# Optimization experiments

Hardware: AMD Instinct MI355X
Metric: run time of the kernel (lower is better)

The kernel has to match this reference:

```python
import jax, jax.numpy as jnp
import numpy as np

B, T, E, H = 8, 2048, 1024, 128

def setup_inputs() -> dict:
    key = jax.random.key(0)
    kx, kq, kk, kv = jax.random.split(key, 4)
    return {
        "X": jax.random.normal(kx, (B, T, E), dtype=jnp.float32),
        "Wq": jax.random.normal(kq, (E, H), dtype=jnp.float32) * (E ** -0.5),
        "Wk": jax.random.normal(kk, (E, H), dtype=jnp.float32) * (E ** -0.5),
        "Wv": jax.random.normal(kv, (E, H), dtype=jnp.float32) * (E ** -0.5),
    }

def reference(X, Wq, Wk, Wv):
    # X: [B, T, E]; Wq/Wk/Wv: [E, H]
    q = X @ Wq  # [B, T, H]
    k = X @ Wk  # [B, T, H]
    v = X @ Wv  # [B, T, H]
    t = X.shape[1]
    scale = float(X.shape[-1]) ** 0.5  # NOTE: source scales by sqrt(embedding_size)
    w = jnp.einsum("bqh,bkh->bqk", q, k) / scale  # [B, T, T]
    mask = jnp.tril(jnp.ones((t, t), dtype=bool))  # causal tril buffer
    w = jnp.where(mask[None, :, :], w, -jnp.inf)
    # NOTE: source applies softmax over dim=1 (the query axis), faithfully reproduced
    w = jax.nn.softmax(w, axis=1)
    # dropout p=0.0 -> identity
    return jnp.einsum("bqk,bkh->bqh", w, v)  # [B, T, H]
```

## Files before the change

### kernel.cpp

```cpp
#include <hip/hip_runtime.h>
#include <hip/hip_bf16.h>
#include <stdint.h>

#define B_ 8
#define T_ 2048
#define E_ 1024
#define H_ 128
#define BT_ (B_*T_)

typedef unsigned short u16;
typedef unsigned int u32;
typedef __attribute__((ext_vector_type(4))) unsigned short u16x4;
typedef __attribute__((ext_vector_type(8))) short short8;
typedef __attribute__((ext_vector_type(4))) float f32x4;

#define MFMA_BF16(a,b,c) __builtin_amdgcn_mfma_f32_16x16x32_bf16((a),(b),(c),0,0,0)

#define SBAR() do { __builtin_amdgcn_sched_barrier(0); __builtin_amdgcn_s_barrier(); __builtin_amdgcn_sched_barrier(0); } while(0)
#define WAITL0() asm volatile("s_waitcnt lgkmcnt(0)" ::: "memory")

__device__ __forceinline__ u16 bf16u(float f) {
  union { float f; unsigned u; } v; v.f = f;
  unsigned r = v.u + 0x7FFFu + ((v.u >> 16) & 1u);
  return (u16)(r >> 16);
}
__device__ __forceinline__ float ubf16(u16 u) {
  union { unsigned u; float f; } v; v.u = ((unsigned)u) << 16; return v.f;
}

__device__ __forceinline__ void gl16(const void* g, void* l) {
  __builtin_amdgcn_global_load_lds(
      (const __attribute__((address_space(1))) void*)g,
      (__attribute__((address_space(3))) void*)l, 16, 0, 0);
}

template<int R, int CB, bool SWZ>
__device__ __forceinline__ void stage_tile(const char* g, int gstride, char* lds) {
  const int lane = threadIdx.x & 63;
  const int wid  = threadIdx.x >> 6;
  constexpr int LPR   = CB / 16;
  constexpr int RPC   = 1024 / CB;
  constexpr int CALLS = (R * CB) / 1024;
  constexpr int CPW   = CALLS / 4;
#pragma unroll
  for (int c = 0; c < CPW; ++c) {
    const int call = wid * CPW + c;
    const int r0   = call * RPC;
    const int row  = r0 + lane / LPR;
    int s = lane % LPR;
    if (SWZ) s = s ^ (row & 7);
    gl16(g + (size_t)row * gstride + s * 16, lds + (size_t)r0 * CB);
  }
}

__device__ __forceinline__ short8 fragr(const u16* lds, int row, int colu16, int CBu) {
  const int slot = (colu16 >> 3) ^ (row & 7);
  return *(const short8*)&lds[(size_t)row * CBu + (slot << 3)];
}

__global__ void k_prep(const float* __restrict__ X, u16* __restrict__ Xb,
                       const float* __restrict__ Wq, const float* __restrict__ Wk,
                       const float* __restrict__ Wv, u16* __restrict__ Wt,
                       float* __restrict__ colsum) {
  const int gidx = blockIdx.x * 256 + threadIdx.x;
  const int n4 = BT_ * E_ / 4;
  for (int i = gidx; i < n4; i += gridDim.x * 256) {
    float4 v = ((const float4*)X)[i];
    u16x4 o;
    o.x = bf16u(v.x); o.y = bf16u(v.y); o.z = bf16u(v.z); o.w = bf16u(v.w);
    ((u16x4*)Xb)[i] = o;
  }
  if (gidx < BT_) colsum[gidx] = 0.f;
  if (gidx < 384 * 1024) {
    int r = gidx >> 10;
    int e = gidx & 1023;
    int i = r >> 7;
    int h = r & 127;
    const float* W = (i == 0) ? Wq : (i == 1) ? Wk : Wv;
    float v = W[(size_t)e * 128 + h];
    if (i == 0) v *= 0.03125f;
    Wt[gidx] = bf16u(v);
  }
}

__global__ __launch_bounds__(256) void k_qkv_gemm(const u16* __restrict__ Xb, const u16* __restrict__ Wt,
                                                  u16* __restrict__ Qs, u16* __restrict__ Kb,
                                                  u16* __restrict__ Vt) {
  __shared__ __align__(16) u16 As[2][128 * 64];
  __shared__ __align__(16) u16 Bs[2][128 * 64];
  const int m0   = blockIdx.x * 128;
  const int nsel = blockIdx.y;
  const int n0   = nsel * 128;
  const int lane = threadIdx.x & 63;
  const int wid  = threadIdx.x >> 6;
  const int ln = lane & 15, h4 = lane >> 4;
  const int wm = (wid >> 1) * 64, wn = (wid & 1) * 64;
  f32x4 acc[4][4] = {};

  auto stage = [&](int t, int buf) {
    stage_tile<128, 128, true>((const char*)(Xb + (size_t)m0 * E_ + t * 64), E_ * 2, (char*)As[buf]);
    stage_tile<128, 128, true>((const char*)(Wt + (size_t)n0 * E_ + t * 64), E_ * 2, (char*)Bs[buf]);
  };
  stage(0, 0);
  for (int t = 0; t < 16; ++t) {
    const int cur = t & 1;
    if (t < 15) stage(t + 1, cur ^ 1);
    if (t < 15) asm volatile("s_waitcnt vmcnt(8)" ::: "memory");
    else        asm volatile("s_waitcnt vmcnt(0)" ::: "memory");
    SBAR();
#pragma unroll
    for (int kk = 0; kk < 2; ++kk) {
      short8 a[4], b[4];
#pragma unroll
      for (int mf = 0; mf < 4; ++mf)
        a[mf] = fragr(As[cur], wm + mf * 16 + ln, kk * 32 + h4 * 8, 64);
#pragma unroll
      for (int nf = 0; nf < 4; ++nf)
        b[nf] = fragr(Bs[cur], wn + nf * 16 + ln, kk * 32 + h4 * 8, 64);
#pragma unroll
      for (int mf = 0; mf < 4; ++mf)
#pragma unroll
        for (int nf = 0; nf < 4; ++nf)
          acc[mf][nf] = MFMA_BF16(a[mf], b[nf], acc[mf][nf]);
    }
    WAITL0();
    SBAR();
  }
#pragma unroll
  for (int mf = 0; mf < 4; ++mf)
#pragma unroll
    for (int nf = 0; nf < 4; ++nf)
#pragma unroll
      for (int i = 0; i < 4; ++i) {
        int r = m0 + wm + mf * 16 + h4 * 4 + i;
        int c = wn + nf * 16 + ln;
        u16 u = bf16u(acc[mf][nf][i]);
        if (nsel == 0)      Qs[(size_t)r * H_ + c] = u;
        else if (nsel == 1) Kb[(size_t)r * H_ + c] = u;
        else {
          int bb = r >> 11, tt = r & (T_ - 1);
          Vt[((size_t)bb * H_ + c) * T_ + tt] = u;
        }
      }
}

__global__ __launch_bounds__(256) void k_score(const u16* __restrict__ Qs, const u16* __restrict__ Kb,
                                               u16* __restrict__ P, float* __restrict__ colsum) {
  __shared__ __align__(16) u16 Kf[128 * 128];
  const int c = blockIdx.x, a = blockIdx.y, b = blockIdx.z;
  const int lo = (c * 17) >> 3, hi = ((c + 1) * 17) >> 3;
  const int lane = threadIdx.x & 63, wid = threadIdx.x >> 6;
  const int ln = lane & 15, h4 = lane >> 4;
  const int wq0 = wid * 32;
  const bool evenlane = !(ln & 1);
  int curqt = -1;
  short8 qa[2][4];
  for (int t = lo; t < hi; ++t) {
    const int qt = (t <= a) ? a : 15 - a;
    const int kt = (t <= a) ? t : t - (a + 1);
    stage_tile<128, 256, true>((const char*)(Kb + ((size_t)b * T_ + kt * 128) * H_), H_ * 2, (char*)Kf);
    if (qt != curqt) {
#pragma unroll
      for (int mf = 0; mf < 2; ++mf)
#pragma unroll
        for (int kk = 0; kk < 4; ++kk)
          qa[mf][kk] = *(const short8*)&Qs[((size_t)b * T_ + qt * 128 + wq0 + mf * 16 + ln) * H_ + kk * 32 + h4 * 8];
      curqt = qt;
    }
    asm volatile("s_waitcnt vmcnt(0)" ::: "memory");
    SBAR();

    f32x4 acc[2][8] = {};
#pragma unroll
    for (int kk = 0; kk < 4; ++kk) {
#pragma unroll
      for (int nf = 0; nf < 8; ++nf) {
        short8 bv = fragr(Kf, nf * 16 + ln, kk * 32 + h4 * 8, 128);
#pragma unroll
        for (int mf = 0; mf < 2; ++mf)
          acc[mf][nf] = MFMA_BF16(qa[mf][kk], bv, acc[mf][nf]);
      }
    }

    const bool diag = (qt == kt);
#pragma unroll
    for (int nf = 0; nf < 8; ++nf) {
      float s = 0.f;
      const int k = nf * 16 + ln;
#pragma unroll
      for (int mf = 0; mf < 2; ++mf) {
#pragma unroll
        for (int i = 0; i < 4; ++i) {
          const int q = wq0 + mf * 16 + h4 * 4 + i;
          float w = __expf(acc[mf][nf][i]);
          if (diag && q < k) w = 0.f;
          acc[mf][nf][i] = w;
          s += w;
        }
      }
      s += __shfl_xor(s, 16);
      s += __shfl_xor(s, 32);
      if (h4 == 0) atomicAdd(&colsum[(size_t)b * T_ + kt * 128 + nf * 16 + ln], s);
    }

    u16* ptile = P + (((size_t)b * 136 + (size_t)qt * (qt + 1) / 2 + kt) << 14);
#pragma unroll
    for (int mf = 0; mf < 2; ++mf)
#pragma unroll
      for (int nf = 0; nf < 8; ++nf) {
        f32x4 v = acc[mf][nf];
        f32x4 pv_;
#pragma unroll
        for (int i = 0; i < 4; ++i) pv_[i] = __shfl_xor(v[i], 1);
#pragma unroll
        for (int j = 0; j < 2; ++j) {
          const int i = evenlane ? j : (2 + j);
          const float flo = evenlane ? v[i] : pv_[i];
          const float fhh = evenlane ? pv_[i] : v[i];
          const u32 pk = (u32)bf16u(flo) | ((u32)bf16u(fhh) << 16);
          const int row = wq0 + mf * 16 + h4 * 4 + i;
          const int kc  = nf * 16 + (ln & ~1);
          *(u32*)((char*)ptile + row * 256 + kc * 2) = pk;
        }
      }
    WAITL0();
    SBAR();
  }
}

__global__ void k_finalize_v(const float* __restrict__ colsum, u16* __restrict__ Vt) {
  const int i8 = blockIdx.x * 256 + threadIdx.x;
  const int b  = i8 >> 15;
  const int r  = i8 & 32767;
  const int h  = r >> 8;
  const int t8 = r & 255;
  u16* p = Vt + ((size_t)b * H_ + h) * T_ + t8 * 8;
  const float* csp = colsum + (size_t)b * T_ + t8 * 8;
  short8 v = *(short8*)p;
  short8 o;
#pragma unroll
  for (int j = 0; j < 8; ++j) {
    float f = ubf16((u16)v[j]) / csp[j];
    o[j] = (short)bf16u(f);
  }
  *(short8*)p = o;
}

__global__ __launch_bounds__(256) void k_pv(const u16* __restrict__ P, const u16* __restrict__ Vt,
                                            float* __restrict__ out) {
  __shared__ __align__(16) u16 Pt[2][128 * 128];
  __shared__ __align__(16) u16 Vs[2][16 * 128];
  const int id = blockIdx.x;
  const int hq = id >> 6;
  const int b  = (id >> 3) & 7;
  const int a  = id & 7;
  const int lane = threadIdx.x & 63, wid = threadIdx.x >> 6;
  const int ln = lane & 15, h4 = lane >> 4;
  const int wq0 = wid * 32;

  auto stage = [&](int t, int buf) {
    const int qt = (t <= a) ? a : 15 - a;
    const int kt = (t <= a) ? t : t - (a + 1);
    const u16* ptile = P + (((size_t)b * 136 + (size_t)qt * (qt + 1) / 2 + kt) << 14);
    stage_tile<128, 256, true>((const char*)ptile, 256, (char*)Pt[buf]);
    stage_tile<16, 256, true>((const char*)(Vt + ((size_t)b * H_ + hq * 16) * T_ + kt * 128), T_ * 2, (char*)Vs[buf]);
  };

  stage(0, 0);
  f32x4 acc[2] = {};
  for (int t = 0; t < 17; ++t) {
    const int cur = t & 1;
    if (t < 16) stage(t + 1, cur ^ 1);
    if (t < 16) asm volatile("s_waitcnt vmcnt(9)" ::: "memory");
    else        asm volatile("s_waitcnt vmcnt(0)" ::: "memory");
    SBAR();
#pragma unroll
    for (int kk = 0; kk < 4; ++kk) {
      short8 bv = fragr(Vs[cur], ln, kk * 32 + h4 * 8, 128);
#pragma unroll
      for (int mf = 0; mf < 2; ++mf) {
        short8 av = fragr(Pt[cur], wq0 + mf * 16 + ln, kk * 32 + h4 * 8, 128);
        acc[mf] = MFMA_BF16(av, bv, acc[mf]);
      }
    }
    if (t == a || t == 16) {
      const int qt = (t == a) ? a : 15 - a;
#pragma unroll
      for (int mf = 0; mf < 2; ++mf) {
#pragma unroll
        for (int i = 0; i < 4; ++i) {
          const int q = qt * 128 + wq0 + mf * 16 + h4 * 4 + i;
          out[((size_t)b * T_ + q) * H_ + hq * 16 + ln] = acc[mf][i];
        }
        acc[mf] = (f32x4){0.f, 0.f, 0.f, 0.f};
      }
    }
    WAITL0();
    SBAR();
  }
}

extern "C" void kernel_launch(void* const* d_in, const int* in_sizes, int n_in,
                              void* d_out, int out_size, void* d_ws, size_t ws_size,
                              hipStream_t stream) {
  const float* X  = (const float*)d_in[0];
  const float* Wq = (const float*)d_in[1];
  const float* Wk = (const float*)d_in[2];
  const float* Wv = (const float*)d_in[3];
  float* out = (float*)d_out;
  char* ws = (char*)d_ws;

  u16 *Xb, *Wt, *Qs, *Kb, *Vt, *Pb;
  float* colsum;
  if (ws_size >= 82640896ULL) {
    Xb = (u16*)(ws + 0);
    Wt = (u16*)(ws + 33554432);
    Qs = (u16*)(ws + 34340864);
    Kb = (u16*)(ws + 38535168);
    Vt = (u16*)(ws + 42729472);
    colsum = (float*)(ws + 46923776);
    Pb = (u16*)(ws + 46989312);
  } else {
    Qs = (u16*)(ws + 0);
    Kb = (u16*)(ws + 4194304);
    Vt = (u16*)(ws + 8388608);
    colsum = (float*)(ws + 12582912);
    Pb = (u16*)(ws + 12648448);
    Xb = (u16*)(ws + 12648448);
    Wt = (u16*)(ws + 46202880);
  }

  k_prep<<<2048, 256, 0, stream>>>(X, Xb, Wq, Wk, Wv, Wt, colsum);
  k_qkv_gemm<<<dim3(128, 3), 256, 0, stream>>>(Xb, Wt, Qs, Kb, Vt);
  k_score<<<dim3(8, 8, 8), 256, 0, stream>>>(Qs, Kb, Pb, colsum);
  k_finalize_v<<<1024, 256, 0, stream>>>(colsum, Vt);
  k_pv<<<512, 256, 0, stream>>>(Pb, Vt, out);
}
```

Measured before the change: 180.0 us.

## Fuse X bf16 conversion into QKV GEMM and merge attention phases cooperatively

```diff
diff --git a/kernel.cpp b/kernel.cpp
--- a/kernel.cpp
+++ b/kernel.cpp
@@ -1,5 +1,6 @@
 #include <hip/hip_runtime.h>
 #include <hip/hip_bf16.h>
+#include <hip/hip_cooperative_groups.h>
 #include <stdint.h>
 
 #define B_ 8
@@ -58,18 +59,10 @@
   return *(const short8*)&lds[(size_t)row * CBu + (slot << 3)];
 }
 
-__global__ void k_prep(const float* __restrict__ X, u16* __restrict__ Xb,
-                       const float* __restrict__ Wq, const float* __restrict__ Wk,
+__global__ void k_prep(const float* __restrict__ Wq, const float* __restrict__ Wk,
                        const float* __restrict__ Wv, u16* __restrict__ Wt,
                        float* __restrict__ colsum) {
   const int gidx = blockIdx.x * 256 + threadIdx.x;
-  const int n4 = BT_ * E_ / 4;
-  for (int i = gidx; i < n4; i += gridDim.x * 256) {
-    float4 v = ((const float4*)X)[i];
-    u16x4 o;
-    o.x = bf16u(v.x); o.y = bf16u(v.y); o.z = bf16u(v.z); o.w = bf16u(v.w);
-    ((u16x4*)Xb)[i] = o;
-  }
   if (gidx < BT_) colsum[gidx] = 0.f;
   if (gidx < 384 * 1024) {
     int r = gidx >> 10;
@@ -83,71 +76,107 @@
   }
 }
 
-__global__ __launch_bounds__(256) void k_qkv_gemm(const u16* __restrict__ Xb, const u16* __restrict__ Wt,
-                                                  u16* __restrict__ Qs, u16* __restrict__ Kb,
-                                                  u16* __restrict__ Vt) {
-  __shared__ __align__(16) u16 As[2][128 * 64];
-  __shared__ __align__(16) u16 Bs[2][128 * 64];
-  const int m0   = blockIdx.x * 128;
-  const int nsel = blockIdx.y;
-  const int n0   = nsel * 128;
-  const int lane = threadIdx.x & 63;
-  const int wid  = threadIdx.x >> 6;
+__global__ __launch_bounds__(256, 1) void k_qkv(const float* __restrict__ X,
+    const u16* __restrict__ Wt, u16* __restrict__ Qs, u16* __restrict__ Kb,
+    u16* __restrict__ Vt) {
+  __shared__ __align__(16) u16 As[2][64 * 64];
+  __shared__ __align__(16) u16 Bs[2][384 * 64];
+  const int m0 = blockIdx.x * 64;
+  const int tid = threadIdx.x;
+  const int lane = tid & 63, wid = tid >> 6;
   const int ln = lane & 15, h4 = lane >> 4;
-  const int wm = (wid >> 1) * 64, wn = (wid & 1) * 64;
-  f32x4 acc[4][4] = {};
-
-  auto stage = [&](int t, int buf) {
-    stage_tile<128, 128, true>((const char*)(Xb + (size_t)m0 * E_ + t * 64), E_ * 2, (char*)As[buf]);
-    stage_tile<128, 128, true>((const char*)(Wt + (size_t)n0 * E_ + t * 64), E_ * 2, (char*)Bs[buf]);
-  };
-  stage(0, 0);
-  for (int t = 0; t < 16; ++t) {
-    const int cur = t & 1;
-    if (t < 15) stage(t + 1, cur ^ 1);
-    if (t < 15) asm volatile("s_waitcnt vmcnt(8)" ::: "memory");
-    else        asm volatile("s_waitcnt vmcnt(0)" ::: "memory");
-    SBAR();
+  const int wr = (wid >> 1) * 32, wc = (wid & 1) * 192;
+  const int ar_r = tid >> 2, ar_c = tid & 3;
+  const float* xrow = X + (size_t)(m0 + ar_r) * E_ + ar_c * 16;
+  f32x4 acc[2][12] = {};
+  float4 arA[4], arB[4];
+
+  auto issueA = [&](int t, float4* ar) {
+    const float4* src = (const float4*)(xrow + t * 64);
+#pragma unroll
+    for (int j = 0; j < 4; ++j) ar[j] = src[j];
+  };
+  auto writeA = [&](int buf, const float4* ar) {
+    u16 tmp[16];
+#pragma unroll
+    for (int j = 0; j < 4; ++j) {
+      tmp[4*j+0] = bf16u(ar[j].x); tmp[4*j+1] = bf16u(ar[j].y);
+      tmp[4*j+2] = bf16u(ar[j].z); tmp[4*j+3] = bf16u(ar[j].w);
+    }
+    const int s0 = ar_c * 2;
+    u16* base = As[buf] + ar_r * 64;
+    *(short8*)(base + (((s0    ) ^ (ar_r & 7)) << 3)) = *(const short8*)&tmp[0];
+    *(short8*)(base + (((s0 + 1) ^ (ar_r & 7)) << 3)) = *(const short8*)&tmp[8];
+  };
+  auto stageB = [&](int t, int buf) {
+    stage_tile<384, 128, true>((const char*)(Wt + t * 64), 2048, (char*)Bs[buf]);
+  };
+  auto compute = [&](int c) {
 #pragma unroll
     for (int kk = 0; kk < 2; ++kk) {
-      short8 a[4], b[4];
-#pragma unroll
-      for (int mf = 0; mf < 4; ++mf)
-        a[mf] = fragr(As[cur], wm + mf * 16 + ln, kk * 32 + h4 * 8, 64);
-#pragma unroll
-      for (int nf = 0; nf < 4; ++nf)
-        b[nf] = fragr(Bs[cur], wn + nf * 16 + ln, kk * 32 + h4 * 8, 64);
-#pragma unroll
-      for (int mf = 0; mf < 4; ++mf)
-#pragma unroll
-        for (int nf = 0; nf < 4; ++nf)
+      short8 a[2], b[12];
+#pragma unroll
+      for (int mf = 0; mf < 2; ++mf)
+        a[mf] = fragr(As[c], wr + mf * 16 + ln, kk * 32 + h4 * 8, 64);
+#pragma unroll
+      for (int nf = 0; nf < 12; ++nf)
+        b[nf] = fragr(Bs[c], wc + nf * 16 + ln, kk * 32 + h4 * 8, 64);
+#pragma unroll
+      for (int mf = 0; mf < 2; ++mf)
+#pragma unroll
+        for (int nf = 0; nf < 12; ++nf)
           acc[mf][nf] = MFMA_BF16(a[mf], b[nf], acc[mf][nf]);
     }
-    WAITL0();
-    SBAR();
-  }
-#pragma unroll
-  for (int mf = 0; mf < 4; ++mf)
-#pragma unroll
-    for (int nf = 0; nf < 4; ++nf)
+  };
+
+  issueA(0, arA);
+  stageB(0, 0);
+  issueA(1, arB);
+  writeA(0, arA);
+  asm volatile("s_waitcnt vmcnt(4)" ::: "memory");
+  WAITL0(); SBAR();
+
+  auto body = [&](int t, float4* issDst, const float4* cvtSrc) {
+    const int c = t & 1;
+    if (t < 15) stageB(t + 1, c ^ 1);
+    if (t < 14) issueA(t + 2, issDst);
+    compute(c);
+    if (t < 15) {
+      writeA(c ^ 1, cvtSrc);
+      if (t < 14) asm volatile("s_waitcnt vmcnt(4)" ::: "memory");
+      else        asm volatile("s_waitcnt vmcnt(0)" ::: "memory");
+      WAITL0(); SBAR();
+    }
+  };
+  for (int tt = 0; tt < 16; tt += 2) {
+    body(tt,     arA, arB);
+    body(tt + 1, arB, arA);
+  }
+
+#pragma unroll
+  for (int mf = 0; mf < 2; ++mf)
+#pragma unroll
+    for (int nf = 0; nf < 12; ++nf) {
+      const int cg = wc + nf * 16 + ln;
 #pragma unroll
       for (int i = 0; i < 4; ++i) {
-        int r = m0 + wm + mf * 16 + h4 * 4 + i;
-        int c = wn + nf * 16 + ln;
-        u16 u = bf16u(acc[mf][nf][i]);
-        if (nsel == 0)      Qs[(size_t)r * H_ + c] = u;
-        else if (nsel == 1) Kb[(size_t)r * H_ + c] = u;
+        const int r = m0 + wr + mf * 16 + h4 * 4 + i;
+        const u16 u = bf16u(acc[mf][nf][i]);
+        if (cg < 128)      Qs[(size_t)r * H_ + cg] = u;
+        else if (cg < 256) Kb[(size_t)r * H_ + (cg - 128)] = u;
         else {
-          int bb = r >> 11, tt = r & (T_ - 1);
-          Vt[((size_t)bb * H_ + c) * T_ + tt] = u;
+          const int bb = r >> 11, t2 = r & (T_ - 1);
+          Vt[((size_t)bb * H_ + (cg - 256)) * T_ + t2] = u;
         }
       }
-}
-
-__global__ __launch_bounds__(256) void k_score(const u16* __restrict__ Qs, const u16* __restrict__ Kb,
-                                               u16* __restrict__ P, float* __restrict__ colsum) {
-  __shared__ __align__(16) u16 Kf[128 * 128];
-  const int c = blockIdx.x, a = blockIdx.y, b = blockIdx.z;
+    }
+}
+
+
+__device__ void phase_score(int wg, u16* lds, const u16* Qs, const u16* Kb,
+                            u16* P, float* colsum) {
+  u16* Kf = lds;
+  const int c = wg >> 6, a = (wg >> 3) & 7, b = wg & 7;
   const int lo = (c * 17) >> 3, hi = ((c + 1) * 17) >> 3;
   const int lane = threadIdx.x & 63, wid = threadIdx.x >> 6;
   const int ln = lane & 15, h4 = lane >> 4;
@@ -228,32 +257,32 @@
   }
 }
 
-__global__ void k_finalize_v(const float* __restrict__ colsum, u16* __restrict__ Vt) {
-  const int i8 = blockIdx.x * 256 + threadIdx.x;
-  const int b  = i8 >> 15;
-  const int r  = i8 & 32767;
-  const int h  = r >> 8;
-  const int t8 = r & 255;
-  u16* p = Vt + ((size_t)b * H_ + h) * T_ + t8 * 8;
-  const float* csp = colsum + (size_t)b * T_ + t8 * 8;
-  short8 v = *(short8*)p;
-  short8 o;
-#pragma unroll
-  for (int j = 0; j < 8; ++j) {
-    float f = ubf16((u16)v[j]) / csp[j];
-    o[j] = (short)bf16u(f);
-  }
-  *(short8*)p = o;
-}
-
-__global__ __launch_bounds__(256) void k_pv(const u16* __restrict__ P, const u16* __restrict__ Vt,
-                                            float* __restrict__ out) {
-  __shared__ __align__(16) u16 Pt[2][128 * 128];
-  __shared__ __align__(16) u16 Vs[2][16 * 128];
-  const int id = blockIdx.x;
-  const int hq = id >> 6;
-  const int b  = (id >> 3) & 7;
-  const int a  = id & 7;
+__device__ void phase_finalize(int wg, const float* colsum, u16* Vt) {
+  for (int i8 = wg * 256 + threadIdx.x; i8 < BT_ * H_ / 8; i8 += 512 * 256) {
+    const int b  = i8 >> 15;
+    const int r  = i8 & 32767;
+    const int h  = r >> 8;
+    const int t8 = r & 255;
+    u16* p = Vt + ((size_t)b * H_ + h) * T_ + t8 * 8;
+    const float* csp = colsum + (size_t)b * T_ + t8 * 8;
+    short8 v = *(short8*)p;
+    short8 o;
+#pragma unroll
+    for (int j = 0; j < 8; ++j) {
+      float f = ubf16((u16)v[j]) / csp[j];
+      o[j] = (short)bf16u(f);
+    }
+    *(short8*)p = o;
+  }
+}
+
+__device__ void phase_pv(int wg, u16* lds, const u16* P, const u16* Vt,
+                         float* out) {
+  u16* Pt0 = lds;
+  u16* Pt1 = lds + 16384;
+  u16* Vs0 = lds + 32768;
+  u16* Vs1 = lds + 34816;
+  const int hq = wg >> 6, b = (wg >> 3) & 7, a = wg & 7;
   const int lane = threadIdx.x & 63, wid = threadIdx.x >> 6;
   const int ln = lane & 15, h4 = lane >> 4;
   const int wq0 = wid * 32;
@@ -262,8 +291,8 @@
     const int qt = (t <= a) ? a : 15 - a;
     const int kt = (t <= a) ? t : t - (a + 1);
     const u16* ptile = P + (((size_t)b * 136 + (size_t)qt * (qt + 1) / 2 + kt) << 14);
-    stage_tile<128, 256, true>((const char*)ptile, 256, (char*)Pt[buf]);
-    stage_tile<16, 256, true>((const char*)(Vt + ((size_t)b * H_ + hq * 16) * T_ + kt * 128), T_ * 2, (char*)Vs[buf]);
+    stage_tile<128, 256, true>((const char*)ptile, 256, (char*)(buf ? Pt1 : Pt0));
+    stage_tile<16, 256, true>((const char*)(Vt + ((size_t)b * H_ + hq * 16) * T_ + kt * 128), T_ * 2, (char*)(buf ? Vs1 : Vs0));
   };
 
   stage(0, 0);
@@ -274,12 +303,14 @@
     if (t < 16) asm volatile("s_waitcnt vmcnt(9)" ::: "memory");
     else        asm volatile("s_waitcnt vmcnt(0)" ::: "memory");
     SBAR();
+    const u16* Ptc = cur ? Pt1 : Pt0;
+    const u16* Vsc = cur ? Vs1 : Vs0;
 #pragma unroll
     for (int kk = 0; kk < 4; ++kk) {
-      short8 bv = fragr(Vs[cur], ln, kk * 32 + h4 * 8, 128);
+      short8 bv = fragr(Vsc, ln, kk * 32 + h4 * 8, 128);
 #pragma unroll
       for (int mf = 0; mf < 2; ++mf) {
-        short8 av = fragr(Pt[cur], wq0 + mf * 16 + ln, kk * 32 + h4 * 8, 128);
+        short8 av = fragr(Ptc, wq0 + mf * 16 + ln, kk * 32 + h4 * 8, 128);
         acc[mf] = MFMA_BF16(av, bv, acc[mf]);
       }
     }
@@ -298,6 +329,36 @@
     WAITL0();
     SBAR();
   }
+}
+
+__global__ __launch_bounds__(256, 2) void k_fused(const u16* Qs, const u16* Kb,
+    u16* P, float* colsum, u16* Vt, float* out) {
+  __shared__ __align__(16) u16 lds[36864];
+  cooperative_groups::grid_group grid = cooperative_groups::this_grid();
+  const int wg = blockIdx.x;
+  phase_score(wg, lds, Qs, Kb, P, colsum);
+  asm volatile("s_waitcnt vmcnt(0) lgkmcnt(0)" ::: "memory");
+  __threadfence();
+  grid.sync();
+  phase_finalize(wg, colsum, Vt);
+  asm volatile("s_waitcnt vmcnt(0) lgkmcnt(0)" ::: "memory");
+  __threadfence();
+  grid.sync();
+  phase_pv(wg, lds, P, Vt, out);
+}
+
+__global__ __launch_bounds__(256, 2) void k_score_only(const u16* Qs, const u16* Kb,
+    u16* P, float* colsum) {
+  __shared__ __align__(16) u16 lds[16384];
+  phase_score(blockIdx.x, lds, Qs, Kb, P, colsum);
+}
+__global__ void k_finalize_only(const float* colsum, u16* Vt) {
+  phase_finalize(blockIdx.x, colsum, Vt);
+}
+__global__ __launch_bounds__(256, 2) void k_pv_only(const u16* P, const u16* Vt,
+    float* out) {
+  __shared__ __align__(16) u16 lds[36864];
+  phase_pv(blockIdx.x, lds, P, Vt, out);
 }
 
 extern "C" void kernel_launch(void* const* d_in, const int* in_sizes, int n_in,
@@ -310,29 +371,23 @@
   float* out = (float*)d_out;
   char* ws = (char*)d_ws;
 
-  u16 *Xb, *Wt, *Qs, *Kb, *Vt, *Pb;
-  float* colsum;
-  if (ws_size >= 82640896ULL) {
-    Xb = (u16*)(ws + 0);
-    Wt = (u16*)(ws + 33554432);
-    Qs = (u16*)(ws + 34340864);
-    Kb = (u16*)(ws + 38535168);
-    Vt = (u16*)(ws + 42729472);
-    colsum = (float*)(ws + 46923776);
-    Pb = (u16*)(ws + 46989312);
-  } else {
-    Qs = (u16*)(ws + 0);
-    Kb = (u16*)(ws + 4194304);
-    Vt = (u16*)(ws + 8388608);
-    colsum = (float*)(ws + 12582912);
-    Pb = (u16*)(ws + 12648448);
-    Xb = (u16*)(ws + 12648448);
-    Wt = (u16*)(ws + 46202880);
-  }
-
-  k_prep<<<2048, 256, 0, stream>>>(X, Xb, Wq, Wk, Wv, Wt, colsum);
-  k_qkv_gemm<<<dim3(128, 3), 256, 0, stream>>>(Xb, Wt, Qs, Kb, Vt);
-  k_score<<<dim3(8, 8, 8), 256, 0, stream>>>(Qs, Kb, Pb, colsum);
-  k_finalize_v<<<1024, 256, 0, stream>>>(colsum, Vt);
-  k_pv<<<512, 256, 0, stream>>>(Pb, Vt, out);
-}
+  u16*   Wt     = (u16*)(ws + 0);
+  u16*   Qs     = (u16*)(ws + 786432);
+  u16*   Kb     = (u16*)(ws + 4980736);
+  u16*   Vt     = (u16*)(ws + 9175040);
+  float* colsum = (float*)(ws + 13369344);
+  u16*   Pb     = (u16*)(ws + 13434880);
+
+  k_prep<<<1536, 256, 0, stream>>>(Wq, Wk, Wv, Wt, colsum);
+  k_qkv<<<256, 256, 0, stream>>>(X, Wt, Qs, Kb, Vt);
+
+  void* args[6] = { (void*)&Qs, (void*)&Kb, (void*)&Pb, (void*)&colsum,
+                    (void*)&Vt, (void*)&out };
+  hipError_t e = hipLaunchCooperativeKernel((const void*)k_fused, dim3(512),
+                                            dim3(256), args, 0, stream);
+  if (e != hipSuccess) {
+    k_score_only<<<512, 256, 0, stream>>>(Qs, Kb, Pb, colsum);
+    k_finalize_only<<<512, 256, 0, stream>>>(colsum, Vt);
+    k_pv_only<<<512, 256, 0, stream>>>(Pb, Vt, out);
+  }
+}
```

After: 414.5 us. 130% more time.
